# Optimization experiments

Hardware: AMD Instinct MI355X
Metric: run time of the kernel (lower is better)

## Reference

```python
import jax, jax.numpy as jnp
import numpy as np

N_NODES = 50000
N_EDGES = 800000
IN_F = 129
HID = 32
HEADS = 4
N_CLS = 40
NEG_SLOPE = 0.2
BN_EPS = 1e-5


def setup_inputs() -> dict:
    key = jax.random.key(0)
    ks = jax.random.split(key, 16)
    x = jax.random.normal(ks[0], (N_NODES, IN_F), dtype=jnp.float32)
    edge_index = jax.random.randint(ks[1], (2, N_EDGES), 0, N_NODES, dtype=jnp.int64)
    # BatchNorm1d (eval mode: running stats)
    bn_gamma = jax.random.normal(ks[2], (IN_F,), dtype=jnp.float32) * 0.1 + 1.0
    bn_beta = jax.random.normal(ks[3], (IN_F,), dtype=jnp.float32) * 0.1
    bn_mean = jax.random.normal(ks[4], (IN_F,), dtype=jnp.float32) * 0.1
    bn_var = jax.random.uniform(ks[5], (IN_F,), dtype=jnp.float32, minval=0.5, maxval=1.5)
    # GATConv 1: in=129 -> heads*hid
    s1 = 1.0 / np.sqrt(IN_F)
    W1 = jax.random.uniform(ks[6], (IN_F, HEADS * HID), dtype=jnp.float32, minval=-s1, maxval=s1)
    a1_src = jax.random.uniform(ks[7], (HEADS, HID), dtype=jnp.float32, minval=-s1, maxval=s1)
    a1_dst = jax.random.uniform(ks[8], (HEADS, HID), dtype=jnp.float32, minval=-s1, maxval=s1)
    b1 = jnp.zeros((HEADS * HID,), dtype=jnp.float32)
    # GATConv 2: in=heads*hid -> heads*n_cls (concat=True default)
    in2 = HEADS * HID
    s2 = 1.0 / np.sqrt(in2)
    W2 = jax.random.uniform(ks[9], (in2, HEADS * N_CLS), dtype=jnp.float32, minval=-s2, maxval=s2)
    a2_src = jax.random.uniform(ks[10], (HEADS, N_CLS), dtype=jnp.float32, minval=-s2, maxval=s2)
    a2_dst = jax.random.uniform(ks[11], (HEADS, N_CLS), dtype=jnp.float32, minval=-s2, maxval=s2)
    b2 = jnp.zeros((HEADS * N_CLS,), dtype=jnp.float32)
    return {"x": x, "edge_index": edge_index,
            "bn_gamma": bn_gamma, "bn_beta": bn_beta, "bn_mean": bn_mean, "bn_var": bn_var,
            "W1": W1, "a1_src": a1_src, "a1_dst": a1_dst, "b1": b1,
            "W2": W2, "a2_src": a2_src, "a2_dst": a2_dst, "b2": b2}


def gat_conv(x, W, a_src, a_dst, bias, src, dst, num_nodes, heads, out_ch):
    # h: [N, H, C]
    h = (x @ W).reshape(num_nodes, heads, out_ch)
    alpha_s = jnp.einsum('nhc,hc->nh', h, a_src)   # [N, H]
    alpha_d = jnp.einsum('nhc,hc->nh', h, a_dst)   # [N, H]
    e = alpha_s[src] + alpha_d[dst]                # [E, H]
    e = jnp.where(e > 0, e, NEG_SLOPE * e)         # LeakyReLU
    # segment softmax grouped by destination node
    e_max = jax.ops.segment_max(e, dst, num_segments=num_nodes)
    p = jnp.exp(e - e_max[dst])
    denom = jax.ops.segment_sum(p, dst, num_segments=num_nodes)
    alpha = p / denom[dst]                         # [E, H]
    msg = h[src] * alpha[:, :, None]               # [E, H, C]
    out = jax.ops.segment_sum(msg, dst, num_segments=num_nodes)
    return out.reshape(num_nodes, heads * out_ch) + bias


def reference(x, edge_index, bn_gamma, bn_beta, bn_mean, bn_var,
              W1, a1_src, a1_dst, b1, W2, a2_src, a2_dst, b2):
    N = x.shape[0]
    loops = jnp.arange(N, dtype=edge_index.dtype)
    src = jnp.concatenate([edge_index[0], loops])  # add self loops (PyG default)
    dst = jnp.concatenate([edge_index[1], loops])
    # BatchNorm1d eval; dropout is identity in eval
    h = (x - bn_mean) * jax.lax.rsqrt(bn_var + BN_EPS) * bn_gamma + bn_beta
    h = gat_conv(h, W1, a1_src, a1_dst, b1, src, dst, N, HEADS, HID)
    h = jax.nn.elu(h)
    h = gat_conv(h, W2, a2_src, a2_dst, b2, src, dst, N, HEADS, N_CLS)
    return h
```

## Files before the change

### kernel.cpp

```cpp
#include <hip/hip_runtime.h>
#include <hip/hip_fp16.h>

#define N_NODES 50000
#define N_EDGES 800000
#define E_TOT   (N_EDGES + N_NODES)
#define IN_F    129
#define HID     32
#define HEADS   4
#define F1      (HEADS * HID)
#define NCLS    40
#define F2      (HEADS * NCLS)
#define NEG     0.2f
#define BN_EPS  1e-5f
#define SCAN_NB ((N_NODES + 255) / 256)
#define LOG2E   1.4426950408889634f

typedef __attribute__((ext_vector_type(8))) short bf16x8;
typedef __attribute__((ext_vector_type(4))) float f32x4;

#define P1_ELEMS (8 * 4 * 64 * 8)
#define P2_ELEMS (10 * 4 * 64 * 8)

__device__ __forceinline__ unsigned short bf16_rne(float f) {
  unsigned u = __float_as_uint(f);
  u = (u + 0x7FFFu + ((u >> 16) & 1u)) >> 16;
  return (unsigned short)u;
}
__device__ __forceinline__ float bf16_to_f(unsigned short s) {
  return __uint_as_float(((unsigned)s) << 16);
}
__device__ __forceinline__ unsigned pack_f16(float a, float b) {
  __half2 h = __floats2half2_rn(a, b);
  return *reinterpret_cast<unsigned*>(&h);
}
__device__ __forceinline__ float2 unpack_f16(unsigned u) {
  __half2 h = *reinterpret_cast<__half2*>(&u);
  return __half22float2(h);
}

__global__ __launch_bounds__(256) void packw_kernel(
    const float* __restrict__ W1, const float* __restrict__ W2,
    unsigned short* __restrict__ p1h, unsigned short* __restrict__ p1l,
    unsigned short* __restrict__ p2h, unsigned short* __restrict__ p2l) {
  int e = blockIdx.x * 256 + threadIdx.x;
  if (e < P1_ELEMS) {
    int i = e & 7, l = (e >> 3) & 63, c = (e >> 9) & 3, t = e >> 11;
    int k = c * 32 + (l >> 4) * 8 + i;
    int col = t * 16 + (l & 15);
    float v = W1[k * F1 + col];
    unsigned short hi = bf16_rne(v);
    p1h[e] = hi;
    p1l[e] = bf16_rne(v - bf16_to_f(hi));
  }
  int e2 = e - P1_ELEMS;
  if (e2 >= 0 && e2 < P2_ELEMS) {
    int i = e2 & 7, l = (e2 >> 3) & 63, c = (e2 >> 9) & 3, t = e2 >> 11;
    int k = c * 32 + (l >> 4) * 8 + i;
    int col = t * 16 + (l & 15);
    float v = W2[k * F2 + col];
    unsigned short hi = bf16_rne(v);
    p2h[e2] = hi;
    p2l[e2] = bf16_rne(v - bf16_to_f(hi));
  }
}

__global__ __launch_bounds__(256) void gemm1_kernel(
    const float* __restrict__ x,
    const float* __restrict__ bng, const float* __restrict__ bnb,
    const float* __restrict__ bnm, const float* __restrict__ bnv,
    const unsigned short* __restrict__ p1h, const unsigned short* __restrict__ p1l,
    const float* __restrict__ W1, float* __restrict__ h1,
    unsigned* __restrict__ h1b) {
  __shared__ float scale[IN_F], shift[IN_F];
  int tid = threadIdx.x;
  if (tid < IN_F) {
    float sc = bng[tid] * rsqrtf(bnv[tid] + BN_EPS);
    scale[tid] = sc;
    shift[tid] = bnb[tid] - bnm[tid] * sc;
  }
  __syncthreads();
  int lane = tid & 63, wave = tid >> 6;
  int row0 = blockIdx.x * 64 + wave * 16;
  if (row0 >= N_NODES) return;
  int arow = row0 + (lane & 15);
  int arow_c = arow < N_NODES ? arow : N_NODES - 1;
  int kb = (lane >> 4) * 8;
  const float* xr = x + (size_t)arow_c * IN_F;
  bf16x8 ah[4], al[4];
#pragma unroll
  for (int c = 0; c < 4; c++) {
    int k0 = c * 32 + kb;
#pragma unroll
    for (int i = 0; i < 8; i++) {
      float a = xr[k0 + i] * scale[k0 + i] + shift[k0 + i];
      unsigned short hi = bf16_rne(a);
      ah[c][i] = (short)hi;
      al[c][i] = (short)bf16_rne(a - bf16_to_f(hi));
    }
  }
  int crow_base = row0 + (lane >> 4) * 4;
  float atail[4];
#pragma unroll
  for (int r = 0; r < 4; r++) {
    int rr = crow_base + r;
    rr = rr < N_NODES ? rr : N_NODES - 1;
    atail[r] = x[(size_t)rr * IN_F + 128] * scale[128] + shift[128];
  }
  int col0 = lane & 15;
  for (int t = 0; t < 8; t++) {
    f32x4 acc = {0.f, 0.f, 0.f, 0.f};
#pragma unroll
    for (int c = 0; c < 4; c++) {
      bf16x8 bh = *(const bf16x8*)(p1h + ((t * 4 + c) * 64 + lane) * 8);
      bf16x8 bl = *(const bf16x8*)(p1l + ((t * 4 + c) * 64 + lane) * 8);
      acc = __builtin_amdgcn_mfma_f32_16x16x32_bf16(ah[c], bh, acc, 0, 0, 0);
      acc = __builtin_amdgcn_mfma_f32_16x16x32_bf16(al[c], bh, acc, 0, 0, 0);
      acc = __builtin_amdgcn_mfma_f32_16x16x32_bf16(ah[c], bl, acc, 0, 0, 0);
    }
    int col = t * 16 + col0;
    float wtail = W1[128 * F1 + col];
#pragma unroll
    for (int r = 0; r < 4; r++) {
      float fin = acc[r] + atail[r] * wtail;
      float odd = __shfl(fin, lane + 1);
      int rr = crow_base + r;
      if (rr < N_NODES) {
        h1[(size_t)rr * F1 + col] = fin;
        if ((col0 & 1) == 0)
          h1b[(size_t)rr * (F1 / 2) + (col >> 1)] = pack_f16(fin, odd);
      }
    }
  }
}

__global__ __launch_bounds__(256) void gemm2_kernel(
    const float* __restrict__ hin,
    const unsigned short* __restrict__ p2h, const unsigned short* __restrict__ p2l,
    float* __restrict__ h2, unsigned* __restrict__ h2b) {
  int tid = threadIdx.x;
  int lane = tid & 63, wave = tid >> 6;
  int row0 = blockIdx.x * 64 + wave * 16;
  if (row0 >= N_NODES) return;
  int arow = row0 + (lane & 15);
  int arow_c = arow < N_NODES ? arow : N_NODES - 1;
  int kb = (lane >> 4) * 8;
  const float* hr = hin + (size_t)arow_c * F1;
  bf16x8 ah[4], al[4];
#pragma unroll
  for (int c = 0; c < 4; c++) {
    float4 v0 = *(const float4*)(hr + c * 32 + kb);
    float4 v1 = *(const float4*)(hr + c * 32 + kb + 4);
    float av[8] = {v0.x, v0.y, v0.z, v0.w, v1.x, v1.y, v1.z, v1.w};
#pragma unroll
    for (int i = 0; i < 8; i++) {
      unsigned short hi = bf16_rne(av[i]);
      ah[c][i] = (short)hi;
      al[c][i] = (short)bf16_rne(av[i] - bf16_to_f(hi));
    }
  }
  int crow_base = row0 + (lane >> 4) * 4;
  int col0 = lane & 15;
  for (int t = 0; t < 10; t++) {
    f32x4 acc = {0.f, 0.f, 0.f, 0.f};
#pragma unroll
    for (int c = 0; c < 4; c++) {
      bf16x8 bh = *(const bf16x8*)(p2h + ((t * 4 + c) * 64 + lane) * 8);
      bf16x8 bl = *(const bf16x8*)(p2l + ((t * 4 + c) * 64 + lane) * 8);
      acc = __builtin_amdgcn_mfma_f32_16x16x32_bf16(ah[c], bh, acc, 0, 0, 0);
      acc = __builtin_amdgcn_mfma_f32_16x16x32_bf16(al[c], bh, acc, 0, 0, 0);
      acc = __builtin_amdgcn_mfma_f32_16x16x32_bf16(ah[c], bl, acc, 0, 0, 0);
    }
    int col = t * 16 + col0;
#pragma unroll
    for (int r = 0; r < 4; r++) {
      int rr = crow_base + r;
      float odd = __shfl(acc[r], lane + 1);
      if (rr < N_NODES) {
        h2[(size_t)rr * F2 + col] = acc[r];
        if ((lane & 1) == 0)
          h2b[(size_t)rr * (F2 / 2) + (col >> 1)] = pack_f16(acc[r], odd);
      }
    }
  }
}

__global__ __launch_bounds__(256) void alpha1_kernel(
    const float* __restrict__ h1, const float* __restrict__ a_src,
    const float* __restrict__ a_dst, float* __restrict__ as,
    float* __restrict__ ad) {
  int t = blockIdx.x * 256 + threadIdx.x;
  if (t >= N_NODES * HEADS) return;
  int n = t >> 2, h = t & 3;
  const float* hp = h1 + (size_t)n * F1 + h * HID;
  const float* sp = a_src + h * HID;
  const float* dp = a_dst + h * HID;
  float s = 0.f, d = 0.f;
#pragma unroll
  for (int c = 0; c < HID; c++) { float v = hp[c]; s += v * sp[c]; d += v * dp[c]; }
  as[t] = s * LOG2E; ad[t] = d * LOG2E;
}

__global__ __launch_bounds__(256) void alpha2_kernel(
    const float* __restrict__ h2, const float* __restrict__ a_src,
    const float* __restrict__ a_dst, float* __restrict__ as,
    float* __restrict__ ad) {
  int t = blockIdx.x * 256 + threadIdx.x;
  if (t >= N_NODES * HEADS) return;
  int n = t >> 2, h = t & 3;
  const float* hp = h2 + (size_t)n * F2 + h * NCLS;
  const float* sp = a_src + h * NCLS;
  const float* dp = a_dst + h * NCLS;
  float s = 0.f, d = 0.f;
#pragma unroll
  for (int c = 0; c < NCLS; c++) { float v = hp[c]; s += v * sp[c]; d += v * dp[c]; }
  as[t] = s * LOG2E; ad[t] = d * LOG2E;
}

__global__ __launch_bounds__(256) void hist_kernel(
    const int* __restrict__ ei, int* __restrict__ counts) {
  int e = blockIdx.x * 256 + threadIdx.x;
  if (e >= E_TOT) return;
  int dst = (e < N_EDGES) ? ei[N_EDGES + e] : (e - N_EDGES);
  atomicAdd(&counts[dst], 1);
}

__global__ __launch_bounds__(256) void partial_kernel(
    const int* __restrict__ counts, int* __restrict__ bsum) {
  __shared__ int red[4];
  int i = blockIdx.x * 256 + threadIdx.x;
  int v = (i < N_NODES) ? counts[i] : 0;
#pragma unroll
  for (int o = 1; o < 64; o <<= 1) v += __shfl_xor(v, o);
  int lane = threadIdx.x & 63, wave = threadIdx.x >> 6;
  if (lane == 0) red[wave] = v;
  __syncthreads();
  if (threadIdx.x == 0) bsum[blockIdx.x] = red[0] + red[1] + red[2] + red[3];
}

__global__ __launch_bounds__(256) void bscan_kernel(
    const int* __restrict__ bsum, int* __restrict__ bpre) {
  __shared__ int sh[256];
  int t = threadIdx.x;
  int v = (t < SCAN_NB) ? bsum[t] : 0;
  sh[t] = v;
  __syncthreads();
  for (int o = 1; o < 256; o <<= 1) {
    int u = (t >= o) ? sh[t - o] : 0;
    __syncthreads();
    sh[t] += u;
    __syncthreads();
  }
  if (t < SCAN_NB) bpre[t] = sh[t] - v;
}

__global__ __launch_bounds__(256) void scatter_kernel(
    const int* __restrict__ counts, const int* __restrict__ bpre,
    int* __restrict__ offsets, int* __restrict__ fillpos) {
  __shared__ int sh[256];
  int t = threadIdx.x;
  int i = blockIdx.x * 256 + t;
  int v = (i < N_NODES) ? counts[i] : 0;
  sh[t] = v;
  __syncthreads();
  for (int o = 1; o < 256; o <<= 1) {
    int u = (t >= o) ? sh[t - o] : 0;
    __syncthreads();
    sh[t] += u;
    __syncthreads();
  }
  if (i < N_NODES) {
    int excl = bpre[blockIdx.x] + sh[t] - v;
    offsets[i] = excl;
    fillpos[i] = excl;
  }
  if (i == 0) offsets[N_NODES] = E_TOT;
}

__global__ __launch_bounds__(256) void fill_kernel(
    const int* __restrict__ ei, int* __restrict__ fillpos,
    int* __restrict__ csr_src) {
  int e = blockIdx.x * 256 + threadIdx.x;
  if (e >= E_TOT) return;
  int src, dst;
  if (e < N_EDGES) { src = ei[e]; dst = ei[N_EDGES + e]; }
  else { src = dst = e - N_EDGES; }
  int pos = atomicAdd(&fillpos[dst], 1);
  csr_src[pos] = src;
}

__global__ __launch_bounds__(256) void agg1_kernel(
    const unsigned* __restrict__ h1b, const float* __restrict__ as,
    const float* __restrict__ ad, const int* __restrict__ off,
    const int* __restrict__ csr, const float* __restrict__ b1,
    float* __restrict__ out) {
  int gw = (blockIdx.x * blockDim.x + threadIdx.x) >> 6;
  int lane = threadIdx.x & 63;
  if (gw >= N_NODES) return;
  int base = off[gw];
  int deg  = off[gw + 1] - base;
  int h = lane & 3;
  int g = lane >> 4;
  float adh = ad[gw * 4 + h];
  float s = 0.f, acc0 = 0.f, acc1 = 0.f;
  int j = 0;
  for (; j + 8 <= deg; j += 8) {
    int sr[8];
#pragma unroll
    for (int u = 0; u < 8; u++) sr[u] = csr[base + j + u];
    float av[8];
#pragma unroll
    for (int u = 0; u < 8; u++) av[u] = as[sr[u]*4 + h];
    unsigned uv[8];
#pragma unroll
    for (int u = 0; u < 8; u++)
      uv[u] = h1b[(size_t)sr[u] * (F1/2) + lane];
    float w[8];
#pragma unroll
    for (int u = 0; u < 8; u++) {
      float v = av[u] + adh;
      v = fmaxf(v, NEG * v);
      w[u] = __builtin_amdgcn_exp2f(v);
      s += w[u];
    }
#pragma unroll
    for (int u = 0; u < 8; u++) {
      float wg = __shfl(w[u], g);
      float2 xv = unpack_f16(uv[u]);
      acc0 += wg * xv.x;
      acc1 += wg * xv.y;
    }
  }
  for (; j < deg; j++) {
    int src = csr[base + j];
    float v = as[src*4 + h] + adh;
    v = fmaxf(v, NEG * v);
    float w = __builtin_amdgcn_exp2f(v);
    s += w;
    unsigned uv = h1b[(size_t)src * (F1/2) + lane];
    float wg = __shfl(w, g);
    float2 xv = unpack_f16(uv);
    acc0 += wg * xv.x;
    acc1 += wg * xv.y;
  }
  float sg = __shfl(s, g);
  float2 bp = *(const float2*)&b1[2*lane];
  float o0 = acc0 / sg + bp.x;
  float o1 = acc1 / sg + bp.y;
  o0 = o0 > 0.f ? o0 : expm1f(o0);
  o1 = o1 > 0.f ? o1 : expm1f(o1);
  *(float2*)&out[(size_t)gw * F1 + 2*lane] = make_float2(o0, o1);
}

__global__ __launch_bounds__(256) void agg2_kernel(
    const unsigned* __restrict__ h2b, const float* __restrict__ as,
    const float* __restrict__ ad, const int* __restrict__ off,
    const int* __restrict__ csr, const float* __restrict__ b2,
    float* __restrict__ out) {
  int gw = (blockIdx.x * blockDim.x + threadIdx.x) >> 6;
  int lane = threadIdx.x & 63;
  if (gw >= N_NODES) return;
  int base = off[gw];
  int deg  = off[gw + 1] - base;
  int h  = lane & 3;
  int gA = lane / 20;
  bool third = lane < 16;
  float adh = ad[gw * 4 + h];
  float s = 0.f, a0 = 0.f, a1 = 0.f, a2 = 0.f, a3 = 0.f;
  int j = 0;
  for (; j + 8 <= deg; j += 8) {
    int sr[8];
#pragma unroll
    for (int u = 0; u < 8; u++) sr[u] = csr[base + j + u];
    float av[8];
#pragma unroll
    for (int u = 0; u < 8; u++) av[u] = as[sr[u]*4 + h];
    unsigned ua[8], ub[8];
#pragma unroll
    for (int u = 0; u < 8; u++) {
      const unsigned* r = h2b + (size_t)sr[u] * (F2/2);
      ua[u] = r[lane];
      ub[u] = third ? r[64 + lane] : 0u;
    }
    float w[8];
#pragma unroll
    for (int u = 0; u < 8; u++) {
      float v = av[u] + adh;
      v = fmaxf(v, NEG * v);
      w[u] = __builtin_amdgcn_exp2f(v);
      s += w[u];
    }
#pragma unroll
    for (int u = 0; u < 8; u++) {
      float wA = __shfl(w[u], gA);
      float w3 = __shfl(w[u], 3);
      float2 fa = unpack_f16(ua[u]);
      float2 fb = unpack_f16(ub[u]);
      a0 += wA * fa.x;
      a1 += wA * fa.y;
      a2 += w3 * fb.x;
      a3 += w3 * fb.y;
    }
  }
  for (; j < deg; j++) {
    int src = csr[base + j];
    float v = as[src*4 + h] + adh;
    v = fmaxf(v, NEG * v);
    float w = __builtin_amdgcn_exp2f(v);
    s += w;
    const unsigned* r = h2b + (size_t)src * (F2/2);
    unsigned ua = r[lane];
    unsigned ub = third ? r[64 + lane] : 0u;
    float wA = __shfl(w, gA);
    float w3 = __shfl(w, 3);
    float2 fa = unpack_f16(ua);
    float2 fb = unpack_f16(ub);
    a0 += wA * fa.x;
    a1 += wA * fa.y;
    a2 += w3 * fb.x;
    a3 += w3 * fb.y;
  }
  float sA = __shfl(s, gA), s3 = __shfl(s, 3);
  float2 bp = *(const float2*)&b2[2*lane];
  *(float2*)&out[(size_t)gw * F2 + 2*lane] =
      make_float2(a0/sA + bp.x, a1/sA + bp.y);
  if (third) {
    float2 bq = *(const float2*)&b2[128 + 2*lane];
    *(float2*)&out[(size_t)gw * F2 + 128 + 2*lane] =
        make_float2(a2/s3 + bq.x, a3/s3 + bq.y);
  }
}

extern "C" void kernel_launch(void* const* d_in, const int* in_sizes, int n_in,
                              void* d_out, int out_size, void* d_ws, size_t ws_size,
                              hipStream_t stream) {
  const float* x   = (const float*)d_in[0];
  const int*   ei  = (const int*)d_in[1];
  const float* bng = (const float*)d_in[2];
  const float* bnb = (const float*)d_in[3];
  const float* bnm = (const float*)d_in[4];
  const float* bnv = (const float*)d_in[5];
  const float* W1  = (const float*)d_in[6];
  const float* a1s = (const float*)d_in[7];
  const float* a1d = (const float*)d_in[8];
  const float* b1  = (const float*)d_in[9];
  const float* W2  = (const float*)d_in[10];
  const float* a2s = (const float*)d_in[11];
  const float* a2d = (const float*)d_in[12];
  const float* b2  = (const float*)d_in[13];
  float* out = (float*)d_out;

  char* ws = (char*)d_ws;
  size_t p = 0;
  auto alloc = [&](size_t bytes) -> char* {
    char* r = ws + p;
    p += (bytes + 255) & ~(size_t)255;
    return r;
  };
  float* h1   = (float*)alloc(sizeof(float) * (size_t)N_NODES * F1);
  float* h1a  = (float*)alloc(sizeof(float) * (size_t)N_NODES * F1);
  float* h2   = (float*)alloc(sizeof(float) * (size_t)N_NODES * F2);
  unsigned* h1b = (unsigned*)alloc(sizeof(unsigned) * (size_t)N_NODES * (F1/2));
  float* as1  = (float*)alloc(sizeof(float) * (size_t)N_NODES * HEADS);
  float* ad1  = (float*)alloc(sizeof(float) * (size_t)N_NODES * HEADS);
  float* as2  = (float*)alloc(sizeof(float) * (size_t)N_NODES * HEADS);
  float* ad2  = (float*)alloc(sizeof(float) * (size_t)N_NODES * HEADS);
  int* counts = (int*)alloc(sizeof(int) * (N_NODES + 1));
  int* offs   = (int*)alloc(sizeof(int) * (N_NODES + 1));
  int* fpos   = (int*)alloc(sizeof(int) * N_NODES);
  int* bsum   = (int*)alloc(sizeof(int) * SCAN_NB);
  int* bpre   = (int*)alloc(sizeof(int) * SCAN_NB);
  int* csr    = (int*)alloc(sizeof(int) * E_TOT);
  unsigned short* p1h = (unsigned short*)alloc(sizeof(unsigned short) * P1_ELEMS);
  unsigned short* p1l = (unsigned short*)alloc(sizeof(unsigned short) * P1_ELEMS);
  unsigned short* p2h = (unsigned short*)alloc(sizeof(unsigned short) * P2_ELEMS);
  unsigned short* p2l = (unsigned short*)alloc(sizeof(unsigned short) * P2_ELEMS);
  unsigned* h2b = (unsigned*)h1;

  hipMemsetAsync(counts, 0, sizeof(int) * (N_NODES + 1), stream);

  packw_kernel<<<(P1_ELEMS + P2_ELEMS + 255) / 256, 256, 0, stream>>>(
      W1, W2, p1h, p1l, p2h, p2l);

  hist_kernel<<<(E_TOT + 255) / 256, 256, 0, stream>>>(ei, counts);
  partial_kernel<<<SCAN_NB, 256, 0, stream>>>(counts, bsum);
  bscan_kernel<<<1, 256, 0, stream>>>(bsum, bpre);
  scatter_kernel<<<SCAN_NB, 256, 0, stream>>>(counts, bpre, offs, fpos);
  fill_kernel<<<(E_TOT + 255) / 256, 256, 0, stream>>>(ei, fpos, csr);

  int gblocks = (N_NODES + 63) / 64;
  gemm1_kernel<<<gblocks, 256, 0, stream>>>(x, bng, bnb, bnm, bnv, p1h, p1l, W1, h1, h1b);
  alpha1_kernel<<<(N_NODES * HEADS + 255) / 256, 256, 0, stream>>>(h1, a1s, a1d, as1, ad1);
  agg1_kernel<<<(N_NODES + 3) / 4, 256, 0, stream>>>(h1b, as1, ad1, offs, csr, b1, h1a);

  gemm2_kernel<<<gblocks, 256, 0, stream>>>(h1a, p2h, p2l, h2, h2b);
  alpha2_kernel<<<(N_NODES * HEADS + 255) / 256, 256, 0, stream>>>(h2, a2s, a2d, as2, ad2);
  agg2_kernel<<<(N_NODES + 3) / 4, 256, 0, stream>>>(h2b, as2, ad2, offs, csr, b2, out);
}
```

Before: 368.7 us.

## Build CSR via two-level destination bucketing with 16-bit source indices

Replaces the five-kernel CSR build (global histogram, partial sums, block scan, scatter, atomic fill) with three kernels. Edges are first binned into 256-node destination buckets using per-bucket atomic counters. Each bucket is then sorted locally in shared memory with a histogram and scan, and written out as a contiguous CSR segment. Source indices are stored as 16-bit values, which halves the index traffic in both aggregation kernels. The trade-offs are heavy atomic contention on roughly 200 bucket counters and a fixed per-bucket capacity (BCAP) that only holds for near-uniform degree distributions; 16-bit indices also rely on N_NODES < 65536.

```diff
diff --git a/kernel.cpp b/kernel.cpp
--- a/kernel.cpp
+++ b/kernel.cpp
@@ -12,7 +12,8 @@
 #define F2      (HEADS * NCLS)
 #define NEG     0.2f
 #define BN_EPS  1e-5f
-#define SCAN_NB ((N_NODES + 255) / 256)
+#define NB      ((N_NODES + 255) / 256)
+#define BCAP    6144
 #define LOG2E   1.4426950408889634f
 
 typedef __attribute__((ext_vector_type(8))) short bf16x8;
@@ -216,32 +217,24 @@
   as[t] = s * LOG2E; ad[t] = d * LOG2E;
 }
 
-__global__ __launch_bounds__(256) void hist_kernel(
-    const int* __restrict__ ei, int* __restrict__ counts) {
+__global__ __launch_bounds__(256) void bucket_kernel(
+    const int* __restrict__ ei, int* __restrict__ bcnt,
+    unsigned* __restrict__ buck) {
   int e = blockIdx.x * 256 + threadIdx.x;
   if (e >= E_TOT) return;
-  int dst = (e < N_EDGES) ? ei[N_EDGES + e] : (e - N_EDGES);
-  atomicAdd(&counts[dst], 1);
-}
-
-__global__ __launch_bounds__(256) void partial_kernel(
-    const int* __restrict__ counts, int* __restrict__ bsum) {
-  __shared__ int red[4];
-  int i = blockIdx.x * 256 + threadIdx.x;
-  int v = (i < N_NODES) ? counts[i] : 0;
-#pragma unroll
-  for (int o = 1; o < 64; o <<= 1) v += __shfl_xor(v, o);
-  int lane = threadIdx.x & 63, wave = threadIdx.x >> 6;
-  if (lane == 0) red[wave] = v;
-  __syncthreads();
-  if (threadIdx.x == 0) bsum[blockIdx.x] = red[0] + red[1] + red[2] + red[3];
-}
-
-__global__ __launch_bounds__(256) void bscan_kernel(
-    const int* __restrict__ bsum, int* __restrict__ bpre) {
+  int src, dst;
+  if (e < N_EDGES) { src = ei[e]; dst = ei[N_EDGES + e]; }
+  else { src = dst = e - N_EDGES; }
+  int b = dst >> 8;
+  int pos = atomicAdd(&bcnt[b], 1);
+  buck[(size_t)b * BCAP + pos] = ((unsigned)(dst & 255) << 16) | (unsigned)src;
+}
+
+__global__ __launch_bounds__(256) void bucketscan_kernel(
+    const int* __restrict__ bcnt, int* __restrict__ bbase) {
   __shared__ int sh[256];
   int t = threadIdx.x;
-  int v = (t < SCAN_NB) ? bsum[t] : 0;
+  int v = (t < NB) ? bcnt[t] : 0;
   sh[t] = v;
   __syncthreads();
   for (int o = 1; o < 256; o <<= 1) {
@@ -250,48 +243,54 @@
     sh[t] += u;
     __syncthreads();
   }
-  if (t < SCAN_NB) bpre[t] = sh[t] - v;
-}
-
-__global__ __launch_bounds__(256) void scatter_kernel(
-    const int* __restrict__ counts, const int* __restrict__ bpre,
-    int* __restrict__ offsets, int* __restrict__ fillpos) {
-  __shared__ int sh[256];
-  int t = threadIdx.x;
-  int i = blockIdx.x * 256 + t;
-  int v = (i < N_NODES) ? counts[i] : 0;
-  sh[t] = v;
+  if (t < NB) bbase[t] = sh[t] - v;
+}
+
+__global__ __launch_bounds__(256) void build_kernel(
+    const int* __restrict__ bcnt, const int* __restrict__ bbase,
+    const unsigned* __restrict__ buck,
+    int* __restrict__ offs, unsigned short* __restrict__ csr) {
+  __shared__ int hist[256];
+  __shared__ int scanbuf[256];
+  __shared__ unsigned short stage[BCAP];
+  int b = blockIdx.x, t = threadIdx.x;
+  hist[t] = 0;
+  __syncthreads();
+  int cnt = bcnt[b];
+  int base = bbase[b];
+  const unsigned* bp = buck + (size_t)b * BCAP;
+  for (int i = t; i < cnt; i += 256)
+    atomicAdd(&hist[bp[i] >> 16], 1);
+  __syncthreads();
+  int v = hist[t];
+  scanbuf[t] = v;
   __syncthreads();
   for (int o = 1; o < 256; o <<= 1) {
-    int u = (t >= o) ? sh[t - o] : 0;
+    int u = (t >= o) ? scanbuf[t - o] : 0;
     __syncthreads();
-    sh[t] += u;
+    scanbuf[t] += u;
     __syncthreads();
   }
-  if (i < N_NODES) {
-    int excl = bpre[blockIdx.x] + sh[t] - v;
-    offsets[i] = excl;
-    fillpos[i] = excl;
-  }
-  if (i == 0) offsets[N_NODES] = E_TOT;
-}
-
-__global__ __launch_bounds__(256) void fill_kernel(
-    const int* __restrict__ ei, int* __restrict__ fillpos,
-    int* __restrict__ csr_src) {
-  int e = blockIdx.x * 256 + threadIdx.x;
-  if (e >= E_TOT) return;
-  int src, dst;
-  if (e < N_EDGES) { src = ei[e]; dst = ei[N_EDGES + e]; }
-  else { src = dst = e - N_EDGES; }
-  int pos = atomicAdd(&fillpos[dst], 1);
-  csr_src[pos] = src;
+  int excl = scanbuf[t] - v;
+  int node = b * 256 + t;
+  if (node < N_NODES) offs[node] = base + excl;
+  if (b == 0 && t == 0) offs[N_NODES] = E_TOT;
+  hist[t] = excl;
+  __syncthreads();
+  for (int i = t; i < cnt; i += 256) {
+    unsigned rec = bp[i];
+    int p = atomicAdd(&hist[rec >> 16], 1);
+    stage[p] = (unsigned short)(rec & 0xFFFFu);
+  }
+  __syncthreads();
+  for (int i = t; i < cnt; i += 256)
+    csr[base + i] = stage[i];
 }
 
 __global__ __launch_bounds__(256) void agg1_kernel(
     const unsigned* __restrict__ h1b, const float* __restrict__ as,
     const float* __restrict__ ad, const int* __restrict__ off,
-    const int* __restrict__ csr, const float* __restrict__ b1,
+    const unsigned short* __restrict__ csr, const float* __restrict__ b1,
     float* __restrict__ out) {
   int gw = (blockIdx.x * blockDim.x + threadIdx.x) >> 6;
   int lane = threadIdx.x & 63;
@@ -354,7 +353,7 @@
 __global__ __launch_bounds__(256) void agg2_kernel(
     const unsigned* __restrict__ h2b, const float* __restrict__ as,
     const float* __restrict__ ad, const int* __restrict__ off,
-    const int* __restrict__ csr, const float* __restrict__ b2,
+    const unsigned short* __restrict__ csr, const float* __restrict__ b2,
     float* __restrict__ out) {
   int gw = (blockIdx.x * blockDim.x + threadIdx.x) >> 6;
   int lane = threadIdx.x & 63;
@@ -464,28 +463,25 @@
   float* ad1  = (float*)alloc(sizeof(float) * (size_t)N_NODES * HEADS);
   float* as2  = (float*)alloc(sizeof(float) * (size_t)N_NODES * HEADS);
   float* ad2  = (float*)alloc(sizeof(float) * (size_t)N_NODES * HEADS);
-  int* counts = (int*)alloc(sizeof(int) * (N_NODES + 1));
+  int* bcnt   = (int*)alloc(sizeof(int) * NB);
+  int* bbase  = (int*)alloc(sizeof(int) * NB);
+  unsigned* buck = (unsigned*)alloc(sizeof(unsigned) * (size_t)NB * BCAP);
   int* offs   = (int*)alloc(sizeof(int) * (N_NODES + 1));
-  int* fpos   = (int*)alloc(sizeof(int) * N_NODES);
-  int* bsum   = (int*)alloc(sizeof(int) * SCAN_NB);
-  int* bpre   = (int*)alloc(sizeof(int) * SCAN_NB);
-  int* csr    = (int*)alloc(sizeof(int) * E_TOT);
+  unsigned short* csr = (unsigned short*)alloc(sizeof(unsigned short) * E_TOT);
   unsigned short* p1h = (unsigned short*)alloc(sizeof(unsigned short) * P1_ELEMS);
   unsigned short* p1l = (unsigned short*)alloc(sizeof(unsigned short) * P1_ELEMS);
   unsigned short* p2h = (unsigned short*)alloc(sizeof(unsigned short) * P2_ELEMS);
   unsigned short* p2l = (unsigned short*)alloc(sizeof(unsigned short) * P2_ELEMS);
   unsigned* h2b = (unsigned*)h1;
 
-  hipMemsetAsync(counts, 0, sizeof(int) * (N_NODES + 1), stream);
+  hipMemsetAsync(bcnt, 0, sizeof(int) * NB, stream);
 
   packw_kernel<<<(P1_ELEMS + P2_ELEMS + 255) / 256, 256, 0, stream>>>(
       W1, W2, p1h, p1l, p2h, p2l);
 
-  hist_kernel<<<(E_TOT + 255) / 256, 256, 0, stream>>>(ei, counts);
-  partial_kernel<<<SCAN_NB, 256, 0, stream>>>(counts, bsum);
-  bscan_kernel<<<1, 256, 0, stream>>>(bsum, bpre);
-  scatter_kernel<<<SCAN_NB, 256, 0, stream>>>(counts, bpre, offs, fpos);
-  fill_kernel<<<(E_TOT + 255) / 256, 256, 0, stream>>>(ei, fpos, csr);
+  bucket_kernel<<<(E_TOT + 255) / 256, 256, 0, stream>>>(ei, bcnt, buck);
+  bucketscan_kernel<<<1, 256, 0, stream>>>(bcnt, bbase);
+  build_kernel<<<NB, 256, 0, stream>>>(bcnt, bbase, buck, offs, csr);
 
   int gblocks = (N_NODES + 63) / 64;
   gemm1_kernel<<<gblocks, 256, 0, stream>>>(x, bng, bnb, bnm, bnv, p1h, p1l, W1, h1, h1b);
```

New measurement: 803.2 us. 2.18x slower.
